# Kernel tuning notes

Measured on AMD Instinct MI355X. Metric: run time of the kernel, lower is better.

The kernel has to match this reference:

```python
import jax, jax.numpy as jnp
import numpy as np

N_NODES = 100000
N_EDGES = 3200000
N_GRAPHS = 1024
HID = 64
NUM_CLASSES = 21


def setup_inputs() -> dict:
    key = jax.random.key(0)
    ks = jax.random.split(key, 12)
    x = jax.random.normal(ks[0], (N_NODES, 1), dtype=jnp.float32)
    edge_index = jax.random.randint(ks[1], (2, N_EDGES), 0, N_NODES, dtype=jnp.int64)
    batch = jnp.sort(jax.random.randint(ks[2], (N_NODES,), 0, N_GRAPHS, dtype=jnp.int64))
    def lin(k, fan_in, fan_out):
        bound = 1.0 / np.sqrt(fan_in)
        return jax.random.uniform(k, (fan_in, fan_out), jnp.float32, -bound, bound)
    return {
        "x": x,
        "edge_index": edge_index,
        "batch": batch,
        # SAGEConv1: lin_l (on aggregated neighbors, with bias), lin_r (root, no bias)
        "W1l": lin(ks[3], 1, HID), "b1": jnp.zeros((HID,), jnp.float32), "W1r": lin(ks[4], 1, HID),
        # SAGEConv2
        "W2l": lin(ks[5], HID, HID), "b2": jnp.zeros((HID,), jnp.float32), "W2r": lin(ks[6], HID, HID),
        # classifier
        "Wc": lin(ks[7], HID, NUM_CLASSES), "bc": jnp.zeros((NUM_CLASSES,), jnp.float32),
    }


def _sage_conv(x, src, dst, Wl, bl, Wr):
    # mean-aggregate neighbor features: gather from src, scatter-mean to dst
    msg = x[src]                                              # [E, F] gather
    agg = jax.ops.segment_sum(msg, dst, num_segments=N_NODES)  # [N, F]
    cnt = jax.ops.segment_sum(jnp.ones((src.shape[0],), x.dtype), dst, num_segments=N_NODES)
    agg = agg / jnp.maximum(cnt, 1.0)[:, None]
    # out = lin_l(aggr) + lin_r(x)
    return agg @ Wl + bl + x @ Wr


def reference(x, edge_index, batch, W1l, b1, W1r, W2l, b2, W2r, Wc, bc):
    src, dst = edge_index[0], edge_index[1]
    h = jax.nn.relu(_sage_conv(x, src, dst, W1l, b1, W1r))
    h = jax.nn.relu(_sage_conv(h, src, dst, W2l, b2, W2r))
    # global mean pool over graphs
    pooled = jax.ops.segment_sum(h, batch, num_segments=N_GRAPHS)
    gcnt = jax.ops.segment_sum(jnp.ones((h.shape[0],), h.dtype), batch, num_segments=N_GRAPHS)
    pooled = pooled / jnp.maximum(gcnt, 1.0)[:, None]
    return pooled @ Wc + bc
```

## Files before the change

### kernel.cpp

```cpp
#include <hip/hip_runtime.h>

#define N_NODES 100000
#define N_EDGES 3200000
#define N_GRAPHS 1024
#define NCLS 21
#define NBKT 782
#define CAP 4480
#define NB 512
#define CHUNK 6250

typedef short s8v __attribute__((ext_vector_type(8)));
typedef float f4v __attribute__((ext_vector_type(4)));

__device__ __forceinline__ float bf2f(unsigned short u) {
    return __uint_as_float(((unsigned)u) << 16);
}
__device__ __forceinline__ unsigned short f2bf(float f) {
    unsigned u = __float_as_uint(f);
    unsigned r = 0x7fffu + ((u >> 16) & 1u);
    return (unsigned short)((u + r) >> 16);
}
__device__ __forceinline__ float lo2f(unsigned w) { return __uint_as_float(w << 16); }
__device__ __forceinline__ float hi2f(unsigned w) { return __uint_as_float(w & 0xffff0000u); }

__global__ void k_prep(const float* __restrict__ W2l, const float* __restrict__ W2r,
                       unsigned short* __restrict__ wp,
                       const int* __restrict__ batch, int* __restrict__ gstart,
                       int* __restrict__ gcur) {
    if (blockIdx.x < 32) {
        int tid = blockIdx.x * 256 + threadIdx.x;
        int frag = tid >> 9;
        int r = tid & 511;
        int L = r >> 3, j = r & 7;
        int kstep = frag >> 2, nt = frag & 3;
        int k = kstep * 32 + (L >> 4) * 8 + j;
        int n = nt * 16 + (L & 15);
        float val = (k < 64) ? W2l[k * 64 + n] : W2r[(k - 64) * 64 + n];
        wp[tid] = f2bf(val);
    } else if (blockIdx.x < 37) {
        int g = (blockIdx.x - 32) * 256 + threadIdx.x;
        if (g > N_GRAPHS) return;
        if (g == N_GRAPHS) { gstart[N_GRAPHS] = N_NODES; return; }
        int lo = 0, hi = N_NODES;
        while (lo < hi) { int m = (lo + hi) >> 1; if (batch[m] < g) lo = m + 1; else hi = m; }
        gstart[g] = lo;
    } else {
        for (int i = threadIdx.x; i < NBKT; i += 256) gcur[i] = i * CAP;
    }
}

__global__ __launch_bounds__(256) void k_binone(const int* __restrict__ src,
                                                const int* __restrict__ dst,
                                                int* __restrict__ gcur,
                                                unsigned int* __restrict__ bins) {
    __shared__ unsigned int ebuf[CHUNK];
    __shared__ unsigned short bbuf[CHUNK];
    __shared__ int lh[NBKT];
    __shared__ int lbase[NBKT];
    int t = threadIdx.x;
    for (int i = t; i < NBKT; i += 256) lh[i] = 0;
    __syncthreads();
    const int2* s2 = (const int2*)(src + blockIdx.x * CHUNK);
    const int2* d2 = (const int2*)(dst + blockIdx.x * CHUNK);
    for (int i = t; i < CHUNK / 2; i += 256) {
        int2 s = s2[i];
        int2 d = d2[i];
        uint2 pp;
        pp.x = ((unsigned)s.x << 7) | (unsigned)(d.x & 127);
        pp.y = ((unsigned)s.y << 7) | (unsigned)(d.y & 127);
        *(uint2*)(&ebuf[2 * i]) = pp;
        bbuf[2 * i]     = (unsigned short)(d.x >> 7);
        bbuf[2 * i + 1] = (unsigned short)(d.y >> 7);
        atomicAdd(&lh[d.x >> 7], 1);
        atomicAdd(&lh[d.y >> 7], 1);
    }
    __syncthreads();
    for (int i = t; i < NBKT; i += 256)
        lbase[i] = atomicAdd(&gcur[i], lh[i]);
    __syncthreads();
    for (int i = t; i < NBKT; i += 256) lh[i] = lbase[i];
    __syncthreads();
    for (int i = t; i < CHUNK; i += 256) {
        int b = (int)bbuf[i];
        int pos = atomicAdd(&lh[b], 1);
        if (pos < (b + 1) * CAP) bins[pos] = ebuf[i];
    }
}

__global__ __launch_bounds__(256) void k_build(
    const int* __restrict__ gcur, unsigned int* __restrict__ bins,
    int* __restrict__ row, unsigned short* __restrict__ deg,
    const float* __restrict__ x,
    const float* __restrict__ W1l, const float* __restrict__ b1,
    const float* __restrict__ W1r, unsigned short* __restrict__ h1b) {
    __shared__ unsigned int ebuf[CAP];
    __shared__ int hist[128];
    __shared__ int curs[128];
    __shared__ int lds[128];
    __shared__ float t1[128];
    int k = blockIdx.x, t = threadIdx.x;
    int e0 = k * CAP;
    int cnt = min(gcur[k] - e0, CAP);
    if (t < 128) { hist[t] = 0; t1[t] = 0.0f; }
    __syncthreads();
    for (int i = t; i < cnt; i += 256) {
        unsigned p = bins[e0 + i];
        ebuf[i] = p;
        atomicAdd(&hist[p & 127u], 1);
    }
    __syncthreads();
    if (t < 128) lds[t] = hist[t];
    __syncthreads();
    for (int off = 1; off < 128; off <<= 1) {
        int cur = (t < 128) ? lds[t] : 0;
        int add = (t < 128 && t >= off) ? lds[t - off] : 0;
        __syncthreads();
        if (t < 128) lds[t] = cur + add;
        __syncthreads();
    }
    if (t < 128) {
        int run = e0 + lds[t] - hist[t];
        curs[t] = run;
        int n = k * 128 + t;
        if (n < N_NODES) { row[n] = run; deg[n] = (unsigned short)hist[t]; }
    }
    __syncthreads();
    for (int i = t; i < cnt; i += 256) {
        unsigned p = ebuf[i];
        int slot = (int)(p & 127u);
        int pos = atomicAdd(&curs[slot], 1);
        bins[pos] = p >> 7;
        atomicAdd(&t1[slot], x[p >> 7]);
    }
    __syncthreads();
    for (int i = t; i < 128 * 64; i += 256) {
        int slot = i >> 6, f = i & 63;
        int n = k * 128 + slot;
        if (n >= N_NODES) break;
        float a = t1[slot] / fmaxf((float)hist[slot], 1.0f);
        float v = a * W1l[f] + b1[f] + x[n] * W1r[f];
        h1b[(size_t)n * 64 + f] = f2bf(fmaxf(v, 0.0f));
    }
}

__global__ __launch_bounds__(256) void k_gather2(
    const int* __restrict__ row, const unsigned short* __restrict__ deg,
    const unsigned int* __restrict__ csr,
    const unsigned short* __restrict__ h1b,
    unsigned short* __restrict__ agg2b) {
    int gw = (blockIdx.x * 256 + threadIdx.x) >> 6;
    int L = threadIdx.x & 63;
    int fo = L & 7;
    int es = L >> 3;
    int nw = gridDim.x * 4;
    for (int n = gw; n < N_NODES; n += nw) {
        int r0 = row[n];
        int dn = (int)deg[n];
        int r1 = r0 + dn;
        float a0 = 0.f, a1 = 0.f, a2 = 0.f, a3 = 0.f,
              a4 = 0.f, a5 = 0.f, a6 = 0.f, a7 = 0.f;
        int base = r0;
        for (; base + 32 <= r1; base += 32) {
            int sA = (int)csr[base + es];
            int sB = (int)csr[base + 8 + es];
            int sC = (int)csr[base + 16 + es];
            int sD = (int)csr[base + 24 + es];
            uint4 dA = *(const uint4*)(h1b + (size_t)sA * 64 + fo * 8);
            uint4 dB = *(const uint4*)(h1b + (size_t)sB * 64 + fo * 8);
            uint4 dC = *(const uint4*)(h1b + (size_t)sC * 64 + fo * 8);
            uint4 dD = *(const uint4*)(h1b + (size_t)sD * 64 + fo * 8);
            a0 += lo2f(dA.x); a1 += hi2f(dA.x); a2 += lo2f(dA.y); a3 += hi2f(dA.y);
            a4 += lo2f(dA.z); a5 += hi2f(dA.z); a6 += lo2f(dA.w); a7 += hi2f(dA.w);
            a0 += lo2f(dB.x); a1 += hi2f(dB.x); a2 += lo2f(dB.y); a3 += hi2f(dB.y);
            a4 += lo2f(dB.z); a5 += hi2f(dB.z); a6 += lo2f(dB.w); a7 += hi2f(dB.w);
            a0 += lo2f(dC.x); a1 += hi2f(dC.x); a2 += lo2f(dC.y); a3 += hi2f(dC.y);
            a4 += lo2f(dC.z); a5 += hi2f(dC.z); a6 += lo2f(dC.w); a7 += hi2f(dC.w);
            a0 += lo2f(dD.x); a1 += hi2f(dD.x); a2 += lo2f(dD.y); a3 += hi2f(dD.y);
            a4 += lo2f(dD.z); a5 += hi2f(dD.z); a6 += lo2f(dD.w); a7 += hi2f(dD.w);
        }
        for (; base + 16 <= r1; base += 16) {
            int sA = (int)csr[base + es];
            int sB = (int)csr[base + 8 + es];
            uint4 dA = *(const uint4*)(h1b + (size_t)sA * 64 + fo * 8);
            uint4 dB = *(const uint4*)(h1b + (size_t)sB * 64 + fo * 8);
            a0 += lo2f(dA.x); a1 += hi2f(dA.x); a2 += lo2f(dA.y); a3 += hi2f(dA.y);
            a4 += lo2f(dA.z); a5 += hi2f(dA.z); a6 += lo2f(dA.w); a7 += hi2f(dA.w);
            a0 += lo2f(dB.x); a1 += hi2f(dB.x); a2 += lo2f(dB.y); a3 += hi2f(dB.y);
            a4 += lo2f(dB.z); a5 += hi2f(dB.z); a6 += lo2f(dB.w); a7 += hi2f(dB.w);
        }
        for (; base < r1; base += 8) {
            int e = base + es;
            bool act = e < r1;
            int sA = (int)csr[act ? e : r1 - 1];
            uint4 d = *(const uint4*)(h1b + (size_t)sA * 64 + fo * 8);
            unsigned m = act ? 0xffffffffu : 0u;
            d.x &= m; d.y &= m; d.z &= m; d.w &= m;
            a0 += lo2f(d.x); a1 += hi2f(d.x); a2 += lo2f(d.y); a3 += hi2f(d.y);
            a4 += lo2f(d.z); a5 += hi2f(d.z); a6 += lo2f(d.w); a7 += hi2f(d.w);
        }
        {
            bool hi = (es & 4) != 0;
            float s0 = hi ? a0 : a4, s1 = hi ? a1 : a5, s2 = hi ? a2 : a6, s3 = hi ? a3 : a7;
            float r0v = __shfl_xor(s0, 32, 64);
            float r1v = __shfl_xor(s1, 32, 64);
            float r2v = __shfl_xor(s2, 32, 64);
            float r3v = __shfl_xor(s3, 32, 64);
            a0 = (hi ? a4 : a0) + r0v;
            a1 = (hi ? a5 : a1) + r1v;
            a2 = (hi ? a6 : a2) + r2v;
            a3 = (hi ? a7 : a3) + r3v;
        }
        {
            bool hi = (es & 2) != 0;
            float s0 = hi ? a0 : a2, s1 = hi ? a1 : a3;
            float r0v = __shfl_xor(s0, 16, 64);
            float r1v = __shfl_xor(s1, 16, 64);
            a0 = (hi ? a2 : a0) + r0v;
            a1 = (hi ? a3 : a1) + r1v;
        }
        {
            bool hi = (es & 1) != 0;
            float s0 = hi ? a0 : a1;
            float r0v = __shfl_xor(s0, 8, 64);
            a0 = (hi ? a1 : a0) + r0v;
        }
        float inv = 1.0f / fmaxf((float)dn, 1.0f);
        agg2b[(size_t)n * 64 + fo * 8 + es] = f2bf(a0 * inv);
    }
}

__global__ __launch_bounds__(256) void k_gemv_mfma(
    const unsigned short* __restrict__ agg2b, const unsigned short* __restrict__ h1b,
    const unsigned short* __restrict__ wp, const float* __restrict__ b2,
    unsigned short* __restrict__ h2b) {
    int L = threadIdx.x & 63;
    int wid = threadIdx.x >> 6;
    int n0 = blockIdx.x * 64 + wid * 16;
    if (n0 >= N_NODES) return;
    int m = L & 15, q = L >> 4;
    int nrow = min(n0 + m, N_NODES - 1);

#define LOADB(i) s8v B##i = *(const s8v*)(wp + (i) * 512 + L * 8)
    LOADB(0); LOADB(1); LOADB(2); LOADB(3);
    LOADB(4); LOADB(5); LOADB(6); LOADB(7);
    LOADB(8); LOADB(9); LOADB(10); LOADB(11);
    LOADB(12); LOADB(13); LOADB(14); LOADB(15);
#undef LOADB

    const s8v a0 = *(const s8v*)(agg2b + (size_t)nrow * 64 + q * 8);
    const s8v a1 = *(const s8v*)(agg2b + (size_t)nrow * 64 + 32 + q * 8);
    const s8v a2 = *(const s8v*)(h1b   + (size_t)nrow * 64 + q * 8);
    const s8v a3 = *(const s8v*)(h1b   + (size_t)nrow * 64 + 32 + q * 8);

    f4v acc0 = {0.f, 0.f, 0.f, 0.f}, acc1 = acc0, acc2 = acc0, acc3 = acc0;
    acc0 = __builtin_amdgcn_mfma_f32_16x16x32_bf16(a0, B0,  acc0, 0, 0, 0);
    acc0 = __builtin_amdgcn_mfma_f32_16x16x32_bf16(a1, B4,  acc0, 0, 0, 0);
    acc0 = __builtin_amdgcn_mfma_f32_16x16x32_bf16(a2, B8,  acc0, 0, 0, 0);
    acc0 = __builtin_amdgcn_mfma_f32_16x16x32_bf16(a3, B12, acc0, 0, 0, 0);
    acc1 = __builtin_amdgcn_mfma_f32_16x16x32_bf16(a0, B1,  acc1, 0, 0, 0);
    acc1 = __builtin_amdgcn_mfma_f32_16x16x32_bf16(a1, B5,  acc1, 0, 0, 0);
    acc1 = __builtin_amdgcn_mfma_f32_16x16x32_bf16(a2, B9,  acc1, 0, 0, 0);
    acc1 = __builtin_amdgcn_mfma_f32_16x16x32_bf16(a3, B13, acc1, 0, 0, 0);
    acc2 = __builtin_amdgcn_mfma_f32_16x16x32_bf16(a0, B2,  acc2, 0, 0, 0);
    acc2 = __builtin_amdgcn_mfma_f32_16x16x32_bf16(a1, B6,  acc2, 0, 0, 0);
    acc2 = __builtin_amdgcn_mfma_f32_16x16x32_bf16(a2, B10, acc2, 0, 0, 0);
    acc2 = __builtin_amdgcn_mfma_f32_16x16x32_bf16(a3, B14, acc2, 0, 0, 0);
    acc3 = __builtin_amdgcn_mfma_f32_16x16x32_bf16(a0, B3,  acc3, 0, 0, 0);
    acc3 = __builtin_amdgcn_mfma_f32_16x16x32_bf16(a1, B7,  acc3, 0, 0, 0);
    acc3 = __builtin_amdgcn_mfma_f32_16x16x32_bf16(a2, B11, acc3, 0, 0, 0);
    acc3 = __builtin_amdgcn_mfma_f32_16x16x32_bf16(a3, B15, acc3, 0, 0, 0);

    int fcol = L & 15;
    float bia0 = b2[fcol], bia1 = b2[16 + fcol], bia2 = b2[32 + fcol], bia3 = b2[48 + fcol];
    int rbase = n0 + q * 4;
#pragma unroll
    for (int r = 0; r < 4; r++) {
        int n = rbase + r;
        if (n < N_NODES) {
            size_t o = (size_t)n * 64 + fcol;
            h2b[o]      = f2bf(fmaxf(acc0[r] + bia0, 0.0f));
            h2b[o + 16] = f2bf(fmaxf(acc1[r] + bia1, 0.0f));
            h2b[o + 32] = f2bf(fmaxf(acc2[r] + bia2, 0.0f));
            h2b[o + 48] = f2bf(fmaxf(acc3[r] + bia3, 0.0f));
        }
    }
}

__global__ __launch_bounds__(256) void k_pool3(
    const unsigned short* __restrict__ h2b, const int* __restrict__ gstart,
    float* __restrict__ pooled) {
    int g = (blockIdx.x * 256 + threadIdx.x) >> 6;
    int f = threadIdx.x & 63;
    if (g >= N_GRAPHS) return;
    int ns = gstart[g], ne = gstart[g + 1];
    float s = 0.0f;
    int n = ns;
    for (; n + 3 < ne; n += 4) {
        float v0 = bf2f(h2b[(size_t)(n)     * 64 + f]);
        float v1 = bf2f(h2b[(size_t)(n + 1) * 64 + f]);
        float v2 = bf2f(h2b[(size_t)(n + 2) * 64 + f]);
        float v3 = bf2f(h2b[(size_t)(n + 3) * 64 + f]);
        s += (v0 + v1) + (v2 + v3);
    }
    for (; n < ne; n++) s += bf2f(h2b[(size_t)n * 64 + f]);
    pooled[g * 64 + f] = s / fmaxf((float)(ne - ns), 1.0f);
}

__global__ void k_cls(const float* __restrict__ pooled, const float* __restrict__ Wc,
                      const float* __restrict__ bc, float* __restrict__ out) {
    __shared__ float rowv[64];
    int g = blockIdx.x;
    int f = threadIdx.x;
    rowv[f] = pooled[g * 64 + f];
    __syncthreads();
    if (f < NCLS) {
        float acc = bc[f];
#pragma unroll
        for (int kk = 0; kk < 64; kk++) acc += rowv[kk] * Wc[kk * NCLS + f];
        out[g * NCLS + f] = acc;
    }
}

extern "C" void kernel_launch(void* const* d_in, const int* in_sizes, int n_in,
                              void* d_out, int out_size, void* d_ws, size_t ws_size,
                              hipStream_t stream) {
    const float* x     = (const float*)d_in[0];
    const int*   eidx  = (const int*)d_in[1];
    const int*   batch = (const int*)d_in[2];
    const float* W1l   = (const float*)d_in[3];
    const float* b1    = (const float*)d_in[4];
    const float* W1r   = (const float*)d_in[5];
    const float* W2l   = (const float*)d_in[6];
    const float* b2    = (const float*)d_in[7];
    const float* W2r   = (const float*)d_in[8];
    const float* Wc    = (const float*)d_in[9];
    const float* bc    = (const float*)d_in[10];
    float* out = (float*)d_out;

    const int* src = eidx;
    const int* dst = eidx + N_EDGES;

    char* p = (char*)d_ws;
    unsigned int* bins    = (unsigned int*)p;   p += (size_t)NBKT * CAP * 4;
    unsigned short* h1b   = (unsigned short*)p; p += (size_t)N_NODES * 64 * 2;
    unsigned short* agg2b = (unsigned short*)p; p += (size_t)N_NODES * 64 * 2;
    int* row   = (int*)p;                       p += (size_t)(N_NODES + 1) * 4;
    unsigned short* deg = (unsigned short*)p;   p += (size_t)N_NODES * 2;
    int* gcur  = (int*)p;                       p += NBKT * 4;
    int* gstart= (int*)p;                       p += (N_GRAPHS + 1) * 4;
    unsigned short* wp = (unsigned short*)p;    p += 8192 * 2;
    float* pooled = (float*)p;                  p += (size_t)N_GRAPHS * 64 * 4;

    unsigned short* h2b = (unsigned short*)bins;

    k_prep  <<<38, 256, 0, stream>>>(W2l, W2r, wp, batch, gstart, gcur);
    k_binone<<<NB, 256, 0, stream>>>(src, dst, gcur, bins);
    k_build <<<NBKT, 256, 0, stream>>>(gcur, bins, row, deg, x, W1l, b1, W1r, h1b);

    k_gather2  <<<2048, 256, 0, stream>>>(row, deg, bins, h1b, agg2b);
    k_gemv_mfma<<<(N_NODES + 63) / 64, 256, 0, stream>>>(agg2b, h1b, wp, b2, h2b);
    k_pool3    <<<(N_GRAPHS * 64) / 256, 256, 0, stream>>>(h2b, gstart, pooled);
    k_cls      <<<N_GRAPHS, 64, 0, stream>>>(pooled, Wc, bc, out);
}
```

Baseline: 244.4 us.

## Fuse layer-2 gather with MFMA GEMV and fuse pooling with classifier

Layer-2 neighbor aggregation and the MFMA transform now run in one kernel. Each wave aggregates 16 nodes into a padded LDS tile and feeds that tile straight into the MFMA, so the agg2b buffer no longer makes a global round trip. Pooling and the classifier are merged into one per-graph block, with four waves splitting the node range and reducing through shared memory. This removes two launches and one intermediate buffer. In exchange the gather loses its grid-stride load balancing: each wave now handles a fixed 16 consecutive nodes, giving only about 1563 blocks.

```diff
diff --git a/kernel.cpp b/kernel.cpp
--- a/kernel.cpp
+++ b/kernel.cpp
@@ -8,6 +8,7 @@
 #define CAP 4480
 #define NB 512
 #define CHUNK 6250
+#define TROW 72
 
 typedef short s8v __attribute__((ext_vector_type(8)));
 typedef float f4v __attribute__((ext_vector_type(4)));
@@ -143,17 +144,24 @@
     }
 }
 
-__global__ __launch_bounds__(256) void k_gather2(
+__global__ __launch_bounds__(256) void k_l2f(
     const int* __restrict__ row, const unsigned short* __restrict__ deg,
     const unsigned int* __restrict__ csr,
     const unsigned short* __restrict__ h1b,
-    unsigned short* __restrict__ agg2b) {
-    int gw = (blockIdx.x * 256 + threadIdx.x) >> 6;
+    const unsigned short* __restrict__ wp, const float* __restrict__ b2,
+    unsigned short* __restrict__ h2b) {
+    __shared__ unsigned short tile[4][16 * TROW];
+    int wid = threadIdx.x >> 6;
+    int w = blockIdx.x * 4 + wid;
+    if (w >= N_NODES / 16) return;
     int L = threadIdx.x & 63;
     int fo = L & 7;
     int es = L >> 3;
-    int nw = gridDim.x * 4;
-    for (int n = gw; n < N_NODES; n += nw) {
+    int fown = fo * 8 + es;
+    unsigned short* tw = tile[wid];
+
+    for (int t = 0; t < 16; t++) {
+        int n = w * 16 + t;
         int r0 = row[n];
         int dn = (int)deg[n];
         int r1 = r0 + dn;
@@ -225,20 +233,16 @@
             a0 = (hi ? a1 : a0) + r0v;
         }
         float inv = 1.0f / fmaxf((float)dn, 1.0f);
-        agg2b[(size_t)n * 64 + fo * 8 + es] = f2bf(a0 * inv);
-    }
-}
-
-__global__ __launch_bounds__(256) void k_gemv_mfma(
-    const unsigned short* __restrict__ agg2b, const unsigned short* __restrict__ h1b,
-    const unsigned short* __restrict__ wp, const float* __restrict__ b2,
-    unsigned short* __restrict__ h2b) {
-    int L = threadIdx.x & 63;
-    int wid = threadIdx.x >> 6;
-    int n0 = blockIdx.x * 64 + wid * 16;
-    if (n0 >= N_NODES) return;
+        tw[t * TROW + fown] = f2bf(a0 * inv);
+    }
+
     int m = L & 15, q = L >> 4;
-    int nrow = min(n0 + m, N_NODES - 1);
+    int nrow = w * 16 + m;
+
+    const s8v a0 = *(const s8v*)(tw + m * TROW + q * 8);
+    const s8v a1 = *(const s8v*)(tw + m * TROW + 32 + q * 8);
+    const s8v a2 = *(const s8v*)(h1b + (size_t)nrow * 64 + q * 8);
+    const s8v a3 = *(const s8v*)(h1b + (size_t)nrow * 64 + 32 + q * 8);
 
 #define LOADB(i) s8v B##i = *(const s8v*)(wp + (i) * 512 + L * 8)
     LOADB(0); LOADB(1); LOADB(2); LOADB(3);
@@ -246,11 +250,6 @@
     LOADB(8); LOADB(9); LOADB(10); LOADB(11);
     LOADB(12); LOADB(13); LOADB(14); LOADB(15);
 #undef LOADB
-
-    const s8v a0 = *(const s8v*)(agg2b + (size_t)nrow * 64 + q * 8);
-    const s8v a1 = *(const s8v*)(agg2b + (size_t)nrow * 64 + 32 + q * 8);
-    const s8v a2 = *(const s8v*)(h1b   + (size_t)nrow * 64 + q * 8);
-    const s8v a3 = *(const s8v*)(h1b   + (size_t)nrow * 64 + 32 + q * 8);
 
     f4v acc0 = {0.f, 0.f, 0.f, 0.f}, acc1 = acc0, acc2 = acc0, acc3 = acc0;
     acc0 = __builtin_amdgcn_mfma_f32_16x16x32_bf16(a0, B0,  acc0, 0, 0, 0);
@@ -272,52 +271,49 @@
 
     int fcol = L & 15;
     float bia0 = b2[fcol], bia1 = b2[16 + fcol], bia2 = b2[32 + fcol], bia3 = b2[48 + fcol];
-    int rbase = n0 + q * 4;
+    int rbase = w * 16 + q * 4;
 #pragma unroll
     for (int r = 0; r < 4; r++) {
-        int n = rbase + r;
-        if (n < N_NODES) {
-            size_t o = (size_t)n * 64 + fcol;
-            h2b[o]      = f2bf(fmaxf(acc0[r] + bia0, 0.0f));
-            h2b[o + 16] = f2bf(fmaxf(acc1[r] + bia1, 0.0f));
-            h2b[o + 32] = f2bf(fmaxf(acc2[r] + bia2, 0.0f));
-            h2b[o + 48] = f2bf(fmaxf(acc3[r] + bia3, 0.0f));
-        }
-    }
-}
-
-__global__ __launch_bounds__(256) void k_pool3(
+        size_t o = (size_t)(rbase + r) * 64 + fcol;
+        h2b[o]      = f2bf(fmaxf(acc0[r] + bia0, 0.0f));
+        h2b[o + 16] = f2bf(fmaxf(acc1[r] + bia1, 0.0f));
+        h2b[o + 32] = f2bf(fmaxf(acc2[r] + bia2, 0.0f));
+        h2b[o + 48] = f2bf(fmaxf(acc3[r] + bia3, 0.0f));
+    }
+}
+
+__global__ __launch_bounds__(256) void k_head(
     const unsigned short* __restrict__ h2b, const int* __restrict__ gstart,
-    float* __restrict__ pooled) {
-    int g = (blockIdx.x * 256 + threadIdx.x) >> 6;
+    const float* __restrict__ Wc, const float* __restrict__ bc,
+    float* __restrict__ out) {
+    __shared__ float part[4][64];
+    __shared__ float rowv[64];
+    int g = blockIdx.x;
+    int wid = threadIdx.x >> 6;
     int f = threadIdx.x & 63;
-    if (g >= N_GRAPHS) return;
     int ns = gstart[g], ne = gstart[g + 1];
     float s = 0.0f;
-    int n = ns;
-    for (; n + 3 < ne; n += 4) {
-        float v0 = bf2f(h2b[(size_t)(n)     * 64 + f]);
-        float v1 = bf2f(h2b[(size_t)(n + 1) * 64 + f]);
-        float v2 = bf2f(h2b[(size_t)(n + 2) * 64 + f]);
-        float v3 = bf2f(h2b[(size_t)(n + 3) * 64 + f]);
+    int n = ns + wid;
+    for (; n + 12 < ne; n += 16) {
+        float v0 = bf2f(h2b[(size_t)(n)      * 64 + f]);
+        float v1 = bf2f(h2b[(size_t)(n + 4)  * 64 + f]);
+        float v2 = bf2f(h2b[(size_t)(n + 8)  * 64 + f]);
+        float v3 = bf2f(h2b[(size_t)(n + 12) * 64 + f]);
         s += (v0 + v1) + (v2 + v3);
     }
-    for (; n < ne; n++) s += bf2f(h2b[(size_t)n * 64 + f]);
-    pooled[g * 64 + f] = s / fmaxf((float)(ne - ns), 1.0f);
-}
-
-__global__ void k_cls(const float* __restrict__ pooled, const float* __restrict__ Wc,
-                      const float* __restrict__ bc, float* __restrict__ out) {
-    __shared__ float rowv[64];
-    int g = blockIdx.x;
-    int f = threadIdx.x;
-    rowv[f] = pooled[g * 64 + f];
-    __syncthreads();
-    if (f < NCLS) {
-        float acc = bc[f];
+    for (; n < ne; n += 4) s += bf2f(h2b[(size_t)n * 64 + f]);
+    part[wid][f] = s;
+    __syncthreads();
+    if (threadIdx.x < 64) {
+        float tot = part[0][f] + part[1][f] + part[2][f] + part[3][f];
+        rowv[f] = tot / fmaxf((float)(ne - ns), 1.0f);
+    }
+    __syncthreads();
+    if (threadIdx.x < NCLS) {
+        float acc = bc[threadIdx.x];
 #pragma unroll
-        for (int kk = 0; kk < 64; kk++) acc += rowv[kk] * Wc[kk * NCLS + f];
-        out[g * NCLS + f] = acc;
+        for (int kk = 0; kk < 64; kk++) acc += rowv[kk] * Wc[kk * NCLS + threadIdx.x];
+        out[g * NCLS + threadIdx.x] = acc;
     }
 }
 
@@ -341,24 +337,18 @@
     const int* dst = eidx + N_EDGES;
 
     char* p = (char*)d_ws;
-    unsigned int* bins    = (unsigned int*)p;   p += (size_t)NBKT * CAP * 4;
-    unsigned short* h1b   = (unsigned short*)p; p += (size_t)N_NODES * 64 * 2;
-    unsigned short* agg2b = (unsigned short*)p; p += (size_t)N_NODES * 64 * 2;
+    unsigned int* bins  = (unsigned int*)p;     p += (size_t)NBKT * CAP * 4;
+    unsigned short* h1b = (unsigned short*)p;   p += (size_t)N_NODES * 64 * 2;
+    unsigned short* h2b = (unsigned short*)p;   p += (size_t)N_NODES * 64 * 2;
     int* row   = (int*)p;                       p += (size_t)(N_NODES + 1) * 4;
     unsigned short* deg = (unsigned short*)p;   p += (size_t)N_NODES * 2;
     int* gcur  = (int*)p;                       p += NBKT * 4;
     int* gstart= (int*)p;                       p += (N_GRAPHS + 1) * 4;
     unsigned short* wp = (unsigned short*)p;    p += 8192 * 2;
-    float* pooled = (float*)p;                  p += (size_t)N_GRAPHS * 64 * 4;
-
-    unsigned short* h2b = (unsigned short*)bins;
 
     k_prep  <<<38, 256, 0, stream>>>(W2l, W2r, wp, batch, gstart, gcur);
     k_binone<<<NB, 256, 0, stream>>>(src, dst, gcur, bins);
     k_build <<<NBKT, 256, 0, stream>>>(gcur, bins, row, deg, x, W1l, b1, W1r, h1b);
-
-    k_gather2  <<<2048, 256, 0, stream>>>(row, deg, bins, h1b, agg2b);
-    k_gemv_mfma<<<(N_NODES + 63) / 64, 256, 0, stream>>>(agg2b, h1b, wp, b2, h2b);
-    k_pool3    <<<(N_GRAPHS * 64) / 256, 256, 0, stream>>>(h2b, gstart, pooled);
-    k_cls      <<<N_GRAPHS, 64, 0, stream>>>(pooled, Wc, bc, out);
-}
+    k_l2f   <<<(N_NODES / 16 + 3) / 4, 256, 0, stream>>>(row, deg, bins, h1b, wp, b2, h2b);
+    k_head  <<<N_GRAPHS, 256, 0, stream>>>(h2b, gstart, Wc, bc, out);
+}
```

Result: faster. 228.5 us (-6.5%).
